# Kernel optimization log

Hardware: AMD Instinct MI355X
Metric: run time of the kernel (lower is better)

The kernel has to match this reference:

```python
import jax, jax.numpy as jnp
import numpy as np

B, S, D, H = 2, 2048, 1024, 16
DEPTH = D // H


def setup_inputs() -> dict:
    key = jax.random.key(0)
    ks = jax.random.split(key, 12)
    sc = 1.0 / np.sqrt(D)
    n = lambda k, shp, s=sc: jax.random.normal(k, shp, dtype=jnp.float32) * s
    return {
        "q": jax.random.normal(ks[0], (B, S, D), dtype=jnp.float32),
        "k": jax.random.normal(ks[1], (B, S, D), dtype=jnp.float32),
        "v": jax.random.normal(ks[2], (B, S, D), dtype=jnp.float32),
        # key-padding mask: 1 = masked, 0 = keep (added to logits * -1e9)
        "mask": (jax.random.uniform(ks[3], (B, 1, 1, S)) < 0.1).astype(jnp.float32),
        "wq_w": n(ks[4], (D, D)), "wq_b": jnp.zeros((D,), jnp.float32),
        "wk_w": n(ks[5], (D, D)), "wk_b": jnp.zeros((D,), jnp.float32),
        "wv_w": n(ks[6], (D, D)), "wv_b": jnp.zeros((D,), jnp.float32),
        "dense_w": n(ks[7], (D, D)), "dense_b": jnp.zeros((D,), jnp.float32),
    }


def _split_heads(x, b, s):
    # [B, S, D] -> [B, H, S, depth]
    return x.reshape(b, s, H, DEPTH).transpose(0, 2, 1, 3)


def reference(q, k, v, mask, wq_w, wq_b, wk_w, wk_b, wv_w, wv_b, dense_w, dense_b):
    b, sq, _ = q.shape
    sk = k.shape[1]
    qh = _split_heads(q @ wq_w.T + wq_b, b, sq)
    kh = _split_heads(k @ wk_w.T + wk_b, b, sk)
    vh = _split_heads(v @ wv_w.T + wv_b, b, sk)
    scale = 1.0 / jnp.sqrt(jnp.float32(DEPTH))
    logits = jnp.einsum('bhqd,bhkd->bhqk', qh, kh) * scale  # [B,H,Sq,Sk]
    logits = logits + mask * (-1e9)
    attn = jax.nn.softmax(logits, axis=-1)
    ctx = jnp.einsum('bhqk,bhkd->bhqd', attn, vh)
    ctx = ctx.transpose(0, 2, 1, 3).reshape(b, sq, D)  # concat heads
    out = ctx @ dense_w.T + dense_b
    return out, attn
```

## Files before the change

### kernel.cpp

```cpp
#include <hip/hip_runtime.h>

#define BB 2
#define SS 2048
#define DD 1024
#define HH 16
#define DEPTH 64
#define MTOT (BB*SS)
#define QW 8
#define QBLK (QW*16)
#define NT (SS/64)

using f16 = _Float16;
typedef _Float16 f16x8 __attribute__((ext_vector_type(8)));
typedef _Float16 f16x4 __attribute__((ext_vector_type(4)));
typedef float f32x4 __attribute__((ext_vector_type(4)));

__global__ __launch_bounds__(256) void proj_kernel(
    const float* __restrict__ xq, const float* __restrict__ xk, const float* __restrict__ xv,
    const float* __restrict__ wq, const float* __restrict__ bq,
    const float* __restrict__ wk, const float* __restrict__ bk,
    const float* __restrict__ wv, const float* __restrict__ bv,
    f16* __restrict__ qh, f16* __restrict__ kh, f16* __restrict__ vt)
{
    const int mode = blockIdx.z;
    const float* X    = (mode==0) ? xq : (mode==1) ? xk : xv;
    const float* W    = (mode==0) ? wq : (mode==1) ? wk : wv;
    const float* bias = (mode==0) ? bq : (mode==1) ? bk : bv;

    __shared__ f16 As[128][72];
    __shared__ f16 Bs[128][72];

    const int tid = threadIdx.x;
    const int wave = tid >> 6, lane = tid & 63;
    const int m0 = blockIdx.y * 128, n0 = blockIdx.x * 128;
    const int wm = (wave >> 1) * 64, wn = (wave & 1) * 64;
    const int lrow = lane & 15, lko = (lane >> 4) * 8;

    f32x4 acc[4][4] = {};

    for (int kk = 0; kk < DD; kk += 64) {
        __syncthreads();
        for (int i = 0; i < 8; ++i) {
            int c = tid + i * 256;
            int r = c >> 4, c4 = c & 15;
            f32x4 av = *(const f32x4*)(X + (size_t)(m0 + r) * DD + kk + c4 * 4);
            f32x4 bv4 = *(const f32x4*)(W + (size_t)(n0 + r) * DD + kk + c4 * 4);
            *(f16x4*)&As[r][c4 * 4] = (f16x4){(f16)av[0], (f16)av[1], (f16)av[2], (f16)av[3]};
            *(f16x4*)&Bs[r][c4 * 4] = (f16x4){(f16)bv4[0], (f16)bv4[1], (f16)bv4[2], (f16)bv4[3]};
        }
        __syncthreads();
        for (int kf = 0; kf < 2; ++kf) {
            f16x8 a[4], bf[4];
            for (int i = 0; i < 4; ++i) a[i]  = *(const f16x8*)&As[wm + i*16 + lrow][kf*32 + lko];
            for (int i = 0; i < 4; ++i) bf[i] = *(const f16x8*)&Bs[wn + i*16 + lrow][kf*32 + lko];
            for (int mi = 0; mi < 4; ++mi)
                for (int ni = 0; ni < 4; ++ni)
                    acc[mi][ni] = __builtin_amdgcn_mfma_f32_16x16x32_f16(a[mi], bf[ni], acc[mi][ni], 0, 0, 0);
        }
    }

    const int rbase = (lane >> 4) * 4;
    if (mode == 2) {
        for (int ni = 0; ni < 4; ++ni) {
            int n = n0 + wn + ni * 16 + lrow;
            float bval = bias[n];
            int hh = n >> 6, dep = n & 63;
            for (int mi = 0; mi < 4; ++mi) {
                int m = m0 + wm + mi * 16 + rbase;
                int bb = m >> 11, s = m & 2047;
                f16x4 pk = {(f16)(acc[mi][ni][0] + bval), (f16)(acc[mi][ni][1] + bval),
                            (f16)(acc[mi][ni][2] + bval), (f16)(acc[mi][ni][3] + bval)};
                *(f16x4*)&vt[((size_t)(bb * HH + hh) * DEPTH + dep) * SS + s] = pk;
            }
        }
    } else {
        f16* dst = (mode == 0) ? qh : kh;
        for (int ni = 0; ni < 4; ++ni) {
            int n = n0 + wn + ni * 16 + lrow;
            float bval = bias[n];
            int hh = n >> 6, dep = n & 63;
            for (int mi = 0; mi < 4; ++mi) {
                for (int j = 0; j < 4; ++j) {
                    int m = m0 + wm + mi * 16 + rbase + j;
                    int bb = m >> 11, s = m & 2047;
                    dst[((size_t)(bb * HH + hh) * SS + s) * DEPTH + dep] = (f16)(acc[mi][ni][j] + bval);
                }
            }
        }
    }
}

__global__ __launch_bounds__(512) void attn_kernel(
    const f16* __restrict__ qh, const f16* __restrict__ kh, const f16* __restrict__ vt,
    const float* __restrict__ mask, float* __restrict__ attn_out, f16* __restrict__ ctx)
{
    __shared__ float mlds[SS];
    __shared__ f16 Ks[2][64][72];
    __shared__ f16 Vs[2][64][72];
    __shared__ f16 Pl[QW][16][72];

    const int tid = threadIdx.x, wave = tid >> 6, lane = tid & 63;
    const int L = blockIdx.x;
    const int xcd = L & 7, iw = L >> 3;
    const int bh = xcd * 4 + (iw >> 4);
    const int qb = iw & 15;
    const int b = bh >> 4, h = bh & 15;
    const int q0 = qb * QBLK;
    const int lrow = lane & 15, lko = (lane >> 4) * 8;
    const int rbase = (lane >> 4) * 4;
    const int sr = tid >> 3, sc = (tid & 7) * 8;

    const f16* Qbase = qh + (size_t)bh * SS * DEPTH;
    const f16* Kst = kh + (size_t)bh * SS * DEPTH + (size_t)sr * DEPTH + sc;
    const f16* Vst = vt + (size_t)bh * DEPTH * SS + (size_t)sr * SS + sc;

    for (int i = tid; i < SS; i += 512) mlds[i] = mask[b * SS + i] * -1e9f;

    f16x8 aq[2];
    for (int kf = 0; kf < 2; ++kf)
        aq[kf] = *(const f16x8*)(Qbase + (size_t)(q0 + wave * 16 + lrow) * DEPTH + kf * 32 + lko);

    float s_l[4] = {0.f, 0.f, 0.f, 0.f};
    {
        f16x8 kreg = *(const f16x8*)(Kst);
        *(f16x8*)&Ks[0][sr][sc] = kreg;
        kreg = *(const f16x8*)(Kst + (size_t)64 * DEPTH);
        __syncthreads();
        for (int kt = 0; kt < NT; ++kt) {
            const int cur = kt & 1;
            for (int nf = 0; nf < 4; ++nf) {
                f32x4 a4 = {};
                for (int kf = 0; kf < 2; ++kf) {
                    f16x8 bf = *(const f16x8*)&Ks[cur][nf * 16 + lrow][kf * 32 + lko];
                    a4 = __builtin_amdgcn_mfma_f32_16x16x32_f16(aq[kf], bf, a4, 0, 0, 0);
                }
                float mb = mlds[kt * 64 + nf * 16 + lrow];
                for (int j = 0; j < 4; ++j) s_l[j] += __expf(a4[j] * 0.125f + mb);
            }
            if (kt + 1 < NT) {
                *(f16x8*)&Ks[cur ^ 1][sr][sc] = kreg;
                if (kt + 2 < NT) kreg = *(const f16x8*)(Kst + (size_t)(kt + 2) * 64 * DEPTH);
            }
            __syncthreads();
        }
    }
    for (int j = 0; j < 4; ++j) {
        float s = s_l[j];
        for (int off = 1; off < 16; off <<= 1) s += __shfl_xor(s, off);
        s_l[j] = 1.0f / s;
    }

    f32x4 cacc[4] = {};
    float* arow = attn_out + ((size_t)bh * SS + q0 + wave * 16) * SS;
    {
        f16x8 kreg = *(const f16x8*)(Kst);
        f16x8 vreg = *(const f16x8*)(Vst);
        *(f16x8*)&Ks[0][sr][sc] = kreg;
        *(f16x8*)&Vs[0][sr][sc] = vreg;
        kreg = *(const f16x8*)(Kst + (size_t)64 * DEPTH);
        vreg = *(const f16x8*)(Vst + 64);
        __syncthreads();
        for (int kt = 0; kt < NT; ++kt) {
            const int cur = kt & 1;
            for (int nf = 0; nf < 4; ++nf) {
                f32x4 a4 = {};
                for (int kf = 0; kf < 2; ++kf) {
                    f16x8 bf = *(const f16x8*)&Ks[cur][nf * 16 + lrow][kf * 32 + lko];
                    a4 = __builtin_amdgcn_mfma_f32_16x16x32_f16(aq[kf], bf, a4, 0, 0, 0);
                }
                float mb = mlds[kt * 64 + nf * 16 + lrow];
                for (int j = 0; j < 4; ++j) {
                    float p = __expf(a4[j] * 0.125f + mb) * s_l[j];
                    Pl[wave][rbase + j][nf * 16 + lrow] = (f16)p;
                }
            }
            for (int kf = 0; kf < 2; ++kf) {
                f16x8 pa = *(const f16x8*)&Pl[wave][lrow][kf * 32 + lko];
                for (int nf = 0; nf < 4; ++nf) {
                    f16x8 bv = *(const f16x8*)&Vs[cur][nf * 16 + lrow][kf * 32 + lko];
                    cacc[nf] = __builtin_amdgcn_mfma_f32_16x16x32_f16(pa, bv, cacc[nf], 0, 0, 0);
                }
            }
            for (int i = 0; i < 4; ++i) {
                int r = i * 4 + (lane >> 4);
                f16x4 pv4 = *(const f16x4*)&Pl[wave][r][(lane & 15) * 4];
                f32x4 o = {(float)pv4[0], (float)pv4[1], (float)pv4[2], (float)pv4[3]};
                __builtin_nontemporal_store(o, (f32x4*)&arow[(size_t)r * SS + kt * 64 + (lane & 15) * 4]);
            }
            if (kt + 1 < NT) {
                *(f16x8*)&Ks[cur ^ 1][sr][sc] = kreg;
                *(f16x8*)&Vs[cur ^ 1][sr][sc] = vreg;
                if (kt + 2 < NT) {
                    kreg = *(const f16x8*)(Kst + (size_t)(kt + 2) * 64 * DEPTH);
                    vreg = *(const f16x8*)(Vst + (kt + 2) * 64);
                }
            }
            __syncthreads();
        }
    }
    for (int nf = 0; nf < 4; ++nf)
        for (int j = 0; j < 4; ++j) {
            int qrow = q0 + wave * 16 + rbase + j;
            ctx[((size_t)(b * SS + qrow) * HH + h) * DEPTH + nf * 16 + lrow] = (f16)cacc[nf][j];
        }
}

__global__ __launch_bounds__(256) void dense_kernel(
    const f16* __restrict__ ctx, const float* __restrict__ W,
    const float* __restrict__ bias, float* __restrict__ out)
{
    __shared__ f16 As[128][72];
    __shared__ f16 Bs[128][72];

    const int tid = threadIdx.x;
    const int wave = tid >> 6, lane = tid & 63;
    const int m0 = blockIdx.y * 128, n0 = blockIdx.x * 128;
    const int wm = (wave >> 1) * 64, wn = (wave & 1) * 64;
    const int lrow = lane & 15, lko = (lane >> 4) * 8;

    f32x4 acc[4][4] = {};

    for (int kk = 0; kk < DD; kk += 64) {
        __syncthreads();
        for (int i = 0; i < 4; ++i) {
            int c = tid + i * 256;
            int r = c >> 3, c8 = c & 7;
            *(f16x8*)&As[r][c8 * 8] = *(const f16x8*)(ctx + (size_t)(m0 + r) * DD + kk + c8 * 8);
        }
        for (int i = 0; i < 8; ++i) {
            int c = tid + i * 256;
            int r = c >> 4, c4 = c & 15;
            f32x4 bv4 = *(const f32x4*)(W + (size_t)(n0 + r) * DD + kk + c4 * 4);
            *(f16x4*)&Bs[r][c4 * 4] = (f16x4){(f16)bv4[0], (f16)bv4[1], (f16)bv4[2], (f16)bv4[3]};
        }
        __syncthreads();
        for (int kf = 0; kf < 2; ++kf) {
            f16x8 a[4], bf[4];
            for (int i = 0; i < 4; ++i) a[i]  = *(const f16x8*)&As[wm + i*16 + lrow][kf*32 + lko];
            for (int i = 0; i < 4; ++i) bf[i] = *(const f16x8*)&Bs[wn + i*16 + lrow][kf*32 + lko];
            for (int mi = 0; mi < 4; ++mi)
                for (int ni = 0; ni < 4; ++ni)
                    acc[mi][ni] = __builtin_amdgcn_mfma_f32_16x16x32_f16(a[mi], bf[ni], acc[mi][ni], 0, 0, 0);
        }
    }

    const int rbase = (lane >> 4) * 4;
    for (int ni = 0; ni < 4; ++ni) {
        int n = n0 + wn + ni * 16 + lrow;
        float bval = bias[n];
        for (int mi = 0; mi < 4; ++mi)
            for (int j = 0; j < 4; ++j) {
                int m = m0 + wm + mi * 16 + rbase + j;
                out[(size_t)m * DD + n] = acc[mi][ni][j] + bval;
            }
    }
}

extern "C" void kernel_launch(void* const* d_in, const int* in_sizes, int n_in,
                              void* d_out, int out_size, void* d_ws, size_t ws_size,
                              hipStream_t stream) {
    const float* q       = (const float*)d_in[0];
    const float* k       = (const float*)d_in[1];
    const float* v       = (const float*)d_in[2];
    const float* mask    = (const float*)d_in[3];
    const float* wq_w    = (const float*)d_in[4];
    const float* wq_b    = (const float*)d_in[5];
    const float* wk_w    = (const float*)d_in[6];
    const float* wk_b    = (const float*)d_in[7];
    const float* wv_w    = (const float*)d_in[8];
    const float* wv_b    = (const float*)d_in[9];
    const float* dense_w = (const float*)d_in[10];
    const float* dense_b = (const float*)d_in[11];

    float* out  = (float*)d_out;
    float* attn = out + (size_t)MTOT * DD;

    const size_t NPROJ = (size_t)BB * HH * SS * DEPTH;
    f16* qh  = (f16*)d_ws;
    f16* kh  = qh + NPROJ;
    f16* vt  = kh + NPROJ;
    f16* ctx = vt + NPROJ;

    proj_kernel<<<dim3(8, 32, 3), 256, 0, stream>>>(q, k, v, wq_w, wq_b, wk_w, wk_b,
                                                    wv_w, wv_b, qh, kh, vt);
    attn_kernel<<<dim3(512), 512, 0, stream>>>(qh, kh, vt, mask, attn, ctx);
    dense_kernel<<<dim3(8, 32), 256, 0, stream>>>(ctx, dense_w, dense_b, out);
}
```

Before: 249.7 us.

## Pre-convert inputs to fp16 and use direct global-to-LDS loads with XOR swizzle

Adds a conversion kernel that casts q/k/v and the three projection weights to fp16 once, staging them in the attention-output buffer as scratch before attn_kernel overwrites it. proj_kernel and attn_kernel then use global_load_lds (direct global-to-LDS DMA) into unpadded, XOR-swizzled LDS tiles in place of register-staged loads and padded arrays. The goal is to halve the global read traffic inside the GEMM, avoid converting the same tiles repeatedly, and cut VGPR round-trips for tile staging. The cost is an extra kernel launch plus a full fp32 read and fp16 write pass over the inputs. The proj loop also now syncs twice per k-step with no double buffering.

```diff
diff --git a/kernel.cpp b/kernel.cpp
--- a/kernel.cpp
+++ b/kernel.cpp
@@ -9,57 +9,85 @@
 #define QW 8
 #define QBLK (QW*16)
 #define NT (SS/64)
+#define NPROJ ((size_t)BB*HH*SS*DEPTH)
+#define WSZ   ((size_t)DD*DD)
 
 using f16 = _Float16;
 typedef _Float16 f16x8 __attribute__((ext_vector_type(8)));
 typedef _Float16 f16x4 __attribute__((ext_vector_type(4)));
 typedef float f32x4 __attribute__((ext_vector_type(4)));
 
+#define GLOAD16(g, l) __builtin_amdgcn_global_load_lds(                      \
+    (__attribute__((address_space(1))) const void*)(g),                      \
+    (__attribute__((address_space(3))) void*)(l), 16, 0, 0)
+
+__global__ __launch_bounds__(256) void cvt_kernel(
+    const float* __restrict__ q, const float* __restrict__ k, const float* __restrict__ v,
+    const float* __restrict__ w0, const float* __restrict__ w1, const float* __restrict__ w2,
+    f16* __restrict__ qf, f16* __restrict__ kf, f16* __restrict__ vf,
+    f16* __restrict__ wq, f16* __restrict__ wk, f16* __restrict__ wv)
+{
+    const int z = blockIdx.y;
+    const float* s = z==0?q : z==1?k : z==2?v : z==3?w0 : z==4?w1 : w2;
+    f16*        d = z==0?qf: z==1?kf: z==2?vf: z==3?wq: z==4?wk: wv;
+    const size_t n = (z < 3) ? NPROJ : WSZ;
+    for (size_t i = ((size_t)blockIdx.x * 256 + threadIdx.x) * 8; i < n;
+         i += (size_t)gridDim.x * 256 * 8) {
+        f32x4 a = *(const f32x4*)(s + i);
+        f32x4 b = *(const f32x4*)(s + i + 4);
+        f16x8 o = {(f16)a[0], (f16)a[1], (f16)a[2], (f16)a[3],
+                   (f16)b[0], (f16)b[1], (f16)b[2], (f16)b[3]};
+        *(f16x8*)(d + i) = o;
+    }
+}
+
 __global__ __launch_bounds__(256) void proj_kernel(
-    const float* __restrict__ xq, const float* __restrict__ xk, const float* __restrict__ xv,
-    const float* __restrict__ wq, const float* __restrict__ bq,
-    const float* __restrict__ wk, const float* __restrict__ bk,
-    const float* __restrict__ wv, const float* __restrict__ bv,
+    const f16* __restrict__ qf, const f16* __restrict__ kf, const f16* __restrict__ vf,
+    const f16* __restrict__ wqw, const f16* __restrict__ wkw, const f16* __restrict__ wvw,
+    const float* __restrict__ bq, const float* __restrict__ bk, const float* __restrict__ bv,
     f16* __restrict__ qh, f16* __restrict__ kh, f16* __restrict__ vt)
 {
     const int mode = blockIdx.z;
-    const float* X    = (mode==0) ? xq : (mode==1) ? xk : xv;
-    const float* W    = (mode==0) ? wq : (mode==1) ? wk : wv;
-    const float* bias = (mode==0) ? bq : (mode==1) ? bk : bv;
-
-    __shared__ f16 As[128][72];
-    __shared__ f16 Bs[128][72];
-
-    const int tid = threadIdx.x;
-    const int wave = tid >> 6, lane = tid & 63;
+    const f16* A    = mode==0 ? qf  : mode==1 ? kf  : vf;
+    const f16* Bw   = mode==0 ? wqw : mode==1 ? wkw : wvw;
+    const float* bias = mode==0 ? bq : mode==1 ? bk : bv;
+
+    __shared__ f16 As[128*64];
+    __shared__ f16 Bs[128*64];
+
+    const int tid = threadIdx.x, wave = tid >> 6, lane = tid & 63;
     const int m0 = blockIdx.y * 128, n0 = blockIdx.x * 128;
     const int wm = (wave >> 1) * 64, wn = (wave & 1) * 64;
-    const int lrow = lane & 15, lko = (lane >> 4) * 8;
+    const int lrow = lane & 15, g = lane >> 4;
+    const int sw = lrow & 7;
+    const int srow = tid >> 3;
+    const int schk = (tid & 7) ^ (srow & 7);
 
     f32x4 acc[4][4] = {};
 
     for (int kk = 0; kk < DD; kk += 64) {
-        __syncthreads();
-        for (int i = 0; i < 8; ++i) {
-            int c = tid + i * 256;
-            int r = c >> 4, c4 = c & 15;
-            f32x4 av = *(const f32x4*)(X + (size_t)(m0 + r) * DD + kk + c4 * 4);
-            f32x4 bv4 = *(const f32x4*)(W + (size_t)(n0 + r) * DD + kk + c4 * 4);
-            *(f16x4*)&As[r][c4 * 4] = (f16x4){(f16)av[0], (f16)av[1], (f16)av[2], (f16)av[3]};
-            *(f16x4*)&Bs[r][c4 * 4] = (f16x4){(f16)bv4[0], (f16)bv4[1], (f16)bv4[2], (f16)bv4[3]};
-        }
-        __syncthreads();
-        for (int kf = 0; kf < 2; ++kf) {
+        #pragma unroll
+        for (int i = 0; i < 4; ++i) {
+            GLOAD16(A  + (size_t)(m0 + i*32 + srow) * DD + kk + schk * 8,
+                    &As[i*2048 + wave*512]);
+            GLOAD16(Bw + (size_t)(n0 + i*32 + srow) * DD + kk + schk * 8,
+                    &Bs[i*2048 + wave*512]);
+        }
+        __syncthreads();
+        for (int kf2 = 0; kf2 < 2; ++kf2) {
             f16x8 a[4], bf[4];
-            for (int i = 0; i < 4; ++i) a[i]  = *(const f16x8*)&As[wm + i*16 + lrow][kf*32 + lko];
-            for (int i = 0; i < 4; ++i) bf[i] = *(const f16x8*)&Bs[wn + i*16 + lrow][kf*32 + lko];
+            for (int i = 0; i < 4; ++i)
+                a[i]  = *(const f16x8*)&As[(wm + i*16 + lrow)*64 + ((kf2*4 + g) ^ sw)*8];
+            for (int i = 0; i < 4; ++i)
+                bf[i] = *(const f16x8*)&Bs[(wn + i*16 + lrow)*64 + ((kf2*4 + g) ^ sw)*8];
             for (int mi = 0; mi < 4; ++mi)
                 for (int ni = 0; ni < 4; ++ni)
                     acc[mi][ni] = __builtin_amdgcn_mfma_f32_16x16x32_f16(a[mi], bf[ni], acc[mi][ni], 0, 0, 0);
         }
-    }
-
-    const int rbase = (lane >> 4) * 4;
+        __syncthreads();
+    }
+
+    const int rbase = g * 4;
     if (mode == 2) {
         for (int ni = 0; ni < 4; ++ni) {
             int n = n0 + wn + ni * 16 + lrow;
@@ -79,13 +107,12 @@
             int n = n0 + wn + ni * 16 + lrow;
             float bval = bias[n];
             int hh = n >> 6, dep = n & 63;
-            for (int mi = 0; mi < 4; ++mi) {
+            for (int mi = 0; mi < 4; ++mi)
                 for (int j = 0; j < 4; ++j) {
                     int m = m0 + wm + mi * 16 + rbase + j;
                     int bb = m >> 11, s = m & 2047;
                     dst[((size_t)(bb * HH + hh) * SS + s) * DEPTH + dep] = (f16)(acc[mi][ni][j] + bval);
                 }
-            }
         }
     }
 }
@@ -95,8 +122,8 @@
     const float* __restrict__ mask, float* __restrict__ attn_out, f16* __restrict__ ctx)
 {
     __shared__ float mlds[SS];
-    __shared__ f16 Ks[2][64][72];
-    __shared__ f16 Vs[2][64][72];
+    __shared__ f16 Ks[2][64*64];
+    __shared__ f16 Vs[2][64*64];
     __shared__ f16 Pl[QW][16][72];
 
     const int tid = threadIdx.x, wave = tid >> 6, lane = tid & 63;
@@ -106,43 +133,39 @@
     const int qb = iw & 15;
     const int b = bh >> 4, h = bh & 15;
     const int q0 = qb * QBLK;
-    const int lrow = lane & 15, lko = (lane >> 4) * 8;
-    const int rbase = (lane >> 4) * 4;
-    const int sr = tid >> 3, sc = (tid & 7) * 8;
+    const int lrow = lane & 15, g = lane >> 4;
+    const int rbase = g * 4;
+    const int sw = lrow & 7;
+    const int srow = tid >> 3;
+    const int schk = (tid & 7) ^ (srow & 7);
 
     const f16* Qbase = qh + (size_t)bh * SS * DEPTH;
-    const f16* Kst = kh + (size_t)bh * SS * DEPTH + (size_t)sr * DEPTH + sc;
-    const f16* Vst = vt + (size_t)bh * DEPTH * SS + (size_t)sr * SS + sc;
+    const f16* Kb = kh + (size_t)bh * SS * DEPTH;
+    const f16* Vb = vt + (size_t)bh * DEPTH * SS;
 
     for (int i = tid; i < SS; i += 512) mlds[i] = mask[b * SS + i] * -1e9f;
 
     f16x8 aq[2];
-    for (int kf = 0; kf < 2; ++kf)
-        aq[kf] = *(const f16x8*)(Qbase + (size_t)(q0 + wave * 16 + lrow) * DEPTH + kf * 32 + lko);
+    for (int kf2 = 0; kf2 < 2; ++kf2)
+        aq[kf2] = *(const f16x8*)(Qbase + (size_t)(q0 + wave*16 + lrow) * DEPTH + kf2*32 + g*8);
 
     float s_l[4] = {0.f, 0.f, 0.f, 0.f};
-    {
-        f16x8 kreg = *(const f16x8*)(Kst);
-        *(f16x8*)&Ks[0][sr][sc] = kreg;
-        kreg = *(const f16x8*)(Kst + (size_t)64 * DEPTH);
-        __syncthreads();
-        for (int kt = 0; kt < NT; ++kt) {
-            const int cur = kt & 1;
-            for (int nf = 0; nf < 4; ++nf) {
-                f32x4 a4 = {};
-                for (int kf = 0; kf < 2; ++kf) {
-                    f16x8 bf = *(const f16x8*)&Ks[cur][nf * 16 + lrow][kf * 32 + lko];
-                    a4 = __builtin_amdgcn_mfma_f32_16x16x32_f16(aq[kf], bf, a4, 0, 0, 0);
-                }
-                float mb = mlds[kt * 64 + nf * 16 + lrow];
-                for (int j = 0; j < 4; ++j) s_l[j] += __expf(a4[j] * 0.125f + mb);
-            }
-            if (kt + 1 < NT) {
-                *(f16x8*)&Ks[cur ^ 1][sr][sc] = kreg;
-                if (kt + 2 < NT) kreg = *(const f16x8*)(Kst + (size_t)(kt + 2) * 64 * DEPTH);
-            }
-            __syncthreads();
-        }
+    GLOAD16(Kb + (size_t)(0*64 + srow) * DEPTH + schk * 8, &Ks[0][wave * 512]);
+    __syncthreads();
+    for (int kt = 0; kt < NT; ++kt) {
+        const int cur = kt & 1;
+        if (kt + 1 < NT)
+            GLOAD16(Kb + (size_t)((kt+1)*64 + srow) * DEPTH + schk * 8, &Ks[cur ^ 1][wave * 512]);
+        for (int nf = 0; nf < 4; ++nf) {
+            f32x4 a4 = {};
+            for (int kf2 = 0; kf2 < 2; ++kf2) {
+                f16x8 bf = *(const f16x8*)&Ks[cur][(nf*16 + lrow)*64 + ((kf2*4 + g) ^ sw)*8];
+                a4 = __builtin_amdgcn_mfma_f32_16x16x32_f16(aq[kf2], bf, a4, 0, 0, 0);
+            }
+            float mb = mlds[kt*64 + nf*16 + lrow];
+            for (int j = 0; j < 4; ++j) s_l[j] += __expf(a4[j] * 0.125f + mb);
+        }
+        __syncthreads();
     }
     for (int j = 0; j < 4; ++j) {
         float s = s_l[j];
@@ -152,56 +175,46 @@
 
     f32x4 cacc[4] = {};
     float* arow = attn_out + ((size_t)bh * SS + q0 + wave * 16) * SS;
-    {
-        f16x8 kreg = *(const f16x8*)(Kst);
-        f16x8 vreg = *(const f16x8*)(Vst);
-        *(f16x8*)&Ks[0][sr][sc] = kreg;
-        *(f16x8*)&Vs[0][sr][sc] = vreg;
-        kreg = *(const f16x8*)(Kst + (size_t)64 * DEPTH);
-        vreg = *(const f16x8*)(Vst + 64);
-        __syncthreads();
-        for (int kt = 0; kt < NT; ++kt) {
-            const int cur = kt & 1;
+    GLOAD16(Kb + (size_t)(0*64 + srow) * DEPTH + schk * 8, &Ks[0][wave * 512]);
+    GLOAD16(Vb + (size_t)srow * SS + 0*64 + schk * 8,      &Vs[0][wave * 512]);
+    __syncthreads();
+    for (int kt = 0; kt < NT; ++kt) {
+        const int cur = kt & 1;
+        if (kt + 1 < NT) {
+            GLOAD16(Kb + (size_t)((kt+1)*64 + srow) * DEPTH + schk * 8, &Ks[cur ^ 1][wave * 512]);
+            GLOAD16(Vb + (size_t)srow * SS + (kt+1)*64 + schk * 8,      &Vs[cur ^ 1][wave * 512]);
+        }
+        for (int nf = 0; nf < 4; ++nf) {
+            f32x4 a4 = {};
+            for (int kf2 = 0; kf2 < 2; ++kf2) {
+                f16x8 bf = *(const f16x8*)&Ks[cur][(nf*16 + lrow)*64 + ((kf2*4 + g) ^ sw)*8];
+                a4 = __builtin_amdgcn_mfma_f32_16x16x32_f16(aq[kf2], bf, a4, 0, 0, 0);
+            }
+            float mb = mlds[kt*64 + nf*16 + lrow];
+            for (int j = 0; j < 4; ++j) {
+                float p = __expf(a4[j] * 0.125f + mb) * s_l[j];
+                Pl[wave][rbase + j][nf*16 + lrow] = (f16)p;
+            }
+        }
+        for (int i = 0; i < 4; ++i) {
+            int r = i * 4 + g;
+            f16x4 pv4 = *(const f16x4*)&Pl[wave][r][lrow * 4];
+            f32x4 o = {(float)pv4[0], (float)pv4[1], (float)pv4[2], (float)pv4[3]};
+            __builtin_nontemporal_store(o, (f32x4*)&arow[(size_t)r * SS + kt*64 + lrow*4]);
+        }
+        for (int kf2 = 0; kf2 < 2; ++kf2) {
+            f16x8 pa = *(const f16x8*)&Pl[wave][lrow][kf2*32 + g*8];
             for (int nf = 0; nf < 4; ++nf) {
-                f32x4 a4 = {};
-                for (int kf = 0; kf < 2; ++kf) {
-                    f16x8 bf = *(const f16x8*)&Ks[cur][nf * 16 + lrow][kf * 32 + lko];
-                    a4 = __builtin_amdgcn_mfma_f32_16x16x32_f16(aq[kf], bf, a4, 0, 0, 0);
-                }
-                float mb = mlds[kt * 64 + nf * 16 + lrow];
-                for (int j = 0; j < 4; ++j) {
-                    float p = __expf(a4[j] * 0.125f + mb) * s_l[j];
-                    Pl[wave][rbase + j][nf * 16 + lrow] = (f16)p;
-                }
-            }
-            for (int kf = 0; kf < 2; ++kf) {
-                f16x8 pa = *(const f16x8*)&Pl[wave][lrow][kf * 32 + lko];
-                for (int nf = 0; nf < 4; ++nf) {
-                    f16x8 bv = *(const f16x8*)&Vs[cur][nf * 16 + lrow][kf * 32 + lko];
-                    cacc[nf] = __builtin_amdgcn_mfma_f32_16x16x32_f16(pa, bv, cacc[nf], 0, 0, 0);
-                }
-            }
-            for (int i = 0; i < 4; ++i) {
-                int r = i * 4 + (lane >> 4);
-                f16x4 pv4 = *(const f16x4*)&Pl[wave][r][(lane & 15) * 4];
-                f32x4 o = {(float)pv4[0], (float)pv4[1], (float)pv4[2], (float)pv4[3]};
-                __builtin_nontemporal_store(o, (f32x4*)&arow[(size_t)r * SS + kt * 64 + (lane & 15) * 4]);
-            }
-            if (kt + 1 < NT) {
-                *(f16x8*)&Ks[cur ^ 1][sr][sc] = kreg;
-                *(f16x8*)&Vs[cur ^ 1][sr][sc] = vreg;
-                if (kt + 2 < NT) {
-                    kreg = *(const f16x8*)(Kst + (size_t)(kt + 2) * 64 * DEPTH);
-                    vreg = *(const f16x8*)(Vst + (kt + 2) * 64);
-                }
-            }
-            __syncthreads();
-        }
+                f16x8 bv = *(const f16x8*)&Vs[cur][(nf*16 + lrow)*64 + ((kf2*4 + g) ^ sw)*8];
+                cacc[nf] = __builtin_amdgcn_mfma_f32_16x16x32_f16(pa, bv, cacc[nf], 0, 0, 0);
+            }
+        }
+        __syncthreads();
     }
     for (int nf = 0; nf < 4; ++nf)
         for (int j = 0; j < 4; ++j) {
             int qrow = q0 + wave * 16 + rbase + j;
-            ctx[((size_t)(b * SS + qrow) * HH + h) * DEPTH + nf * 16 + lrow] = (f16)cacc[nf][j];
+            ctx[((size_t)(b * SS + qrow) * HH + h) * DEPTH + nf*16 + lrow] = (f16)cacc[nf][j];
         }
 }
 
@@ -275,14 +288,23 @@
     float* out  = (float*)d_out;
     float* attn = out + (size_t)MTOT * DD;
 
-    const size_t NPROJ = (size_t)BB * HH * SS * DEPTH;
     f16* qh  = (f16*)d_ws;
     f16* kh  = qh + NPROJ;
     f16* vt  = kh + NPROJ;
     f16* ctx = vt + NPROJ;
 
-    proj_kernel<<<dim3(8, 32, 3), 256, 0, stream>>>(q, k, v, wq_w, wq_b, wk_w, wk_b,
-                                                    wv_w, wv_b, qh, kh, vt);
+    f16* sc   = (f16*)attn;
+    f16* qf   = sc;
+    f16* kf   = sc + NPROJ;
+    f16* vf   = sc + 2*NPROJ;
+    f16* wq16 = sc + 3*NPROJ;
+    f16* wk16 = wq16 + WSZ;
+    f16* wv16 = wk16 + WSZ;
+
+    cvt_kernel<<<dim3(1024, 6), 256, 0, stream>>>(q, k, v, wq_w, wk_w, wv_w,
+                                                  qf, kf, vf, wq16, wk16, wv16);
+    proj_kernel<<<dim3(8, 32, 3), 256, 0, stream>>>(qf, kf, vf, wq16, wk16, wv16,
+                                                    wq_b, wk_b, wv_b, qh, kh, vt);
     attn_kernel<<<dim3(512), 512, 0, stream>>>(qh, kh, vt, mask, attn, ctx);
     dense_kernel<<<dim3(8, 32), 256, 0, stream>>>(ctx, dense_w, dense_b, out);
 }
```

Result: faster. 235.3 us (-5.8%).
